# Optimization experiments

Hardware: AMD Instinct MI355X
Metric: run time of the kernel (lower is better)

Reference implementation:

```python
import jax, jax.numpy as jnp
import numpy as np

EPS = 1e-7
N_CAPS_J = 24
ROUTE_MIN = 0.0
N_ITER = 3
INV_TEMP = 0.5
INV_TEMP_DELTA = 0.1


def create_coords_mat(batch, d, h, w, ch, matrix_dim, rel_center=True):
    # Coordinate addition: pad (d,h,w) grid coords to matrix_dim (zeros first).
    subs = (d // 2, h // 2, w // 2) if rel_center else (0, 0, 0)
    f32 = jnp.float32
    dd = jnp.broadcast_to(jnp.arange(d, dtype=f32).reshape(d, 1, 1, 1, 1), (d, h, w, ch, 1)) - subs[0]
    hh = jnp.broadcast_to(jnp.arange(h, dtype=f32).reshape(1, h, 1, 1, 1), (d, h, w, ch, 1)) - subs[1]
    ww = jnp.broadcast_to(jnp.arange(w, dtype=f32).reshape(1, 1, w, 1, 1), (d, h, w, ch, 1)) - subs[2]
    c = jnp.concatenate([dd, hh, ww], -1).reshape(1, d * h * w, ch, 3)
    c = jnp.broadcast_to(c, (batch, d * h * w, ch, 3))
    zeros = jnp.zeros((batch, d * h * w, ch, matrix_dim - 3), dtype=f32)
    return jnp.concatenate([zeros, c], -1)  # (B, dhw, ch, matrix_dim)


def em_routing(v, a_i, beta_v, beta_a):
    # v: (B, Ci, Cj, M) votes; a_i: (B, Ci, 1) input activations.
    B, Ci, Cj, M = v.shape
    a_i = a_i[..., None]  # (B, Ci, 1, 1)

    def stats(r):
        den = r.sum(1, keepdims=True) + EPS                                   # (B,1,Cj,1)
        m = (v * r).sum(1, keepdims=True) / (den + EPS)                       # (B,1,Cj,M)
        s = (r * jnp.square(v - m)).sum(1, keepdims=True) / (den + EPS)       # (B,1,Cj,M)
        cost = ((beta_v + jnp.log(jnp.sqrt(s + EPS) + EPS)) * den).sum(-1, keepdims=True)  # (B,1,Cj,1)
        cm = cost.mean(-2, keepdims=True)
        cs = jnp.sqrt(jnp.square(cost - cm).sum(-2, keepdims=True) / Cj + EPS)
        return m, s, cost, cm, cs

    # Initialization step (uniform assignment scaled by input activations).
    r0 = jnp.full((B, Ci, Cj, 1), 1.0 / Cj, dtype=v.dtype) * a_i
    m, s, cost, cm, cs = stats(r0)
    a_j = jax.nn.sigmoid(INV_TEMP * (beta_a + (cm - cost) / (cs + EPS)))      # (B,1,Cj,1)

    def route(carry, counter):
        mean, stdsqr, act_j, it = carry
        # E-step: Gaussian log-likelihood of each vote under each output capsule.
        expo = (jnp.square(v - mean) / (2.0 * stdsqr + EPS)).sum(-1)          # (B,Ci,Cj)
        coef = -0.5 * jnp.log(2.0 * np.pi * stdsqr + EPS).sum(-1)             # (B,1,Cj)
        log_ap = jnp.log(act_j + EPS).reshape(B, 1, Cj) + coef - expo
        r_ij = jax.nn.softmax(log_ap + EPS, axis=-1)[..., None] * a_i         # (B,Ci,Cj,1)
        # M-step
        m, s, cost, cm, cs = stats(r_ij)
        it = it + counter * INV_TEMP_DELTA
        act = jax.nn.sigmoid(it * (beta_a + (cm - cost) / (cs + EPS)))
        return (m, s, act, it), None

    counters = jnp.arange(1, N_ITER, dtype=v.dtype)  # while_loop runs for counter=1..n_iterations-1
    init = (m, s, a_j, jnp.asarray(INV_TEMP, v.dtype))
    (mean, _, act_j, _), _ = jax.lax.scan(route, init, counters)
    return mean.reshape(B, Cj, M), act_j.reshape(B, Cj, 1)


def setup_inputs() -> dict:
    key = jax.random.key(0)
    k1, k2, k3, k4, k5 = jax.random.split(key, 5)
    B, D, H, W, Ch, M = 4, 4, 14, 14, 32, 16
    J = N_CAPS_J
    pose = jax.random.normal(k1, (B, D, H, W, Ch, M), dtype=jnp.float32)
    activation = jax.random.uniform(k2, (B, D, H, W, Ch, 1), dtype=jnp.float32)
    w = 0.1 * jax.random.normal(k3, (Ch, J, 4, 4), dtype=jnp.float32)
    beta_v = 0.1 * jax.random.normal(k4, (J, M), dtype=jnp.float32)
    beta_a = 0.1 * jax.random.normal(k5, (J, 1), dtype=jnp.float32)
    return {"pose": pose, "activation": activation, "w": w, "beta_v": beta_v, "beta_a": beta_a}


def reference(pose, activation, w, beta_v, beta_a):
    B, D, H, W, Ch, M = pose.shape
    n_i = D * H * W
    sq = int(np.sqrt(M))  # 4x4 pose matrices
    u = pose.reshape(B, n_i, Ch, sq, sq)
    coords = create_coords_mat(B, D, H, W, Ch, M, rel_center=True)            # (B,n_i,Ch,M)
    # Votes: each 4x4 pose matrix times per-(channel, out-capsule) transform.
    votes = jnp.einsum('bicpk,cjkq->bicjpq', u, w).reshape(B, n_i, Ch, N_CAPS_J, M)
    votes = votes + coords[:, :, :, None, :]  # coordinate addition (broadcast over Cj)
    votes = votes.reshape(B, n_i * Ch, N_CAPS_J, M)
    acts = activation.reshape(B, n_i * Ch, 1)
    acts = jnp.where(acts >= ROUTE_MIN, acts, 0.0)
    return em_routing(votes, acts, beta_v, beta_a)
```

## Files before the change

### kernel.cpp

```cpp
#include <hip/hip_runtime.h>
#include <math.h>

#define EPS 1e-7f
#define JC 24
#define CHN 32
#define D_ 4
#define H_ 14
#define W_ 14
#define NI 784
#define CI 25088
#define BATCH 4
#define NP 792
#define ST_STRIDE 792
#define NR 28
#define TWO_PI 6.28318530717958647692f
#define LOG2E 1.44269504088896340736f

__device__ __forceinline__ float groupReduceSum16(float x) {
    x += __shfl_xor(x, 1);
    x += __shfl_xor(x, 2);
    x += __shfl_xor(x, 4);
    x += __shfl_xor(x, 8);
    return x;
}

template<int CTRL>
__device__ __forceinline__ float dpp_mv(float x) {
    return __int_as_float(__builtin_amdgcn_update_dpp(
        0, __float_as_int(x), CTRL, 0xF, 0xF, true));
}

__device__ __forceinline__ float groupSum32_dpp(float x) {
    x += dpp_mv<0xB1>(x);
    x += dpp_mv<0x4E>(x);
    x += dpp_mv<0x141>(x);
    x += dpp_mv<0x140>(x);
    x += __shfl_xor(x, 16);
    return x;
}

template<int PASS, int SPB, int CSEG>
__global__ __launch_bounds__(256, 3)
void accum_kernel(const float* __restrict__ pose, const float* __restrict__ act,
                  const float* __restrict__ w, const float* __restrict__ ST,
                  float* __restrict__ P) {
    __shared__ float w_lds[CSEG * 16 * JC];
    __shared__ float red[4 * JC * 33];

    const int t = threadIdx.x;
    const int h = t >> 5;
    const int jl = t & 31;
    const int jc = jl < 23 ? jl : 23;
    const int b = blockIdx.z;
    const int c0 = blockIdx.y * CSEG;
    const int sp0 = blockIdx.x * SPB;

    for (int idx = t; idx < CSEG * 384; idx += 256) {
        const int cs = idx / 384;
        const int r2 = idx - cs * 384;
        const int jj = r2 >> 4;
        const int kq = r2 & 15;
        w_lds[(cs * 16 + kq) * JC + jj] = w[((size_t)(c0 + cs) * JC + jj) * 16 + kq];
    }

    float SA[16], MS[16], K = 0.f;
    if (PASS) {
        const float* stb = ST + b * ST_STRIDE;
        #pragma unroll
        for (int m4 = 0; m4 < 4; ++m4) {
            float4 a4 = *(const float4*)&stb[jc * 16 + m4 * 4];
            SA[m4*4+0] = a4.x; SA[m4*4+1] = a4.y; SA[m4*4+2] = a4.z; SA[m4*4+3] = a4.w;
            float4 b4 = *(const float4*)&stb[384 + jc * 16 + m4 * 4];
            MS[m4*4+0] = b4.x; MS[m4*4+1] = b4.y; MS[m4*4+2] = b4.z; MS[m4*4+3] = b4.w;
        }
        K = stb[768 + jc];
    }

    float accR = 0.f, accV[16], accV2[16];
    #pragma unroll
    for (int m = 0; m < 16; ++m) { accV[m] = 0.f; accV2[m] = 0.f; }

    __syncthreads();

    #pragma unroll 1
    for (int r = 0; r < SPB / 8; ++r) {
        const int sp = sp0 + r * 8 + h;
        const int dd = sp / (H_ * W_);
        const int rem = sp - dd * (H_ * W_);
        const int hh = rem / W_;
        const int ww = rem - hh * W_;
        const float cd = (float)(dd - D_ / 2);
        const float ch = (float)(hh - H_ / 2);
        const float cw = (float)(ww - W_ / 2);

        const float* upb = pose + (((size_t)b * NI + sp) * CHN + c0) * 16;
        const float* apb = act + ((size_t)b * NI + sp) * CHN + c0;

        float4 pu0 = *(const float4*)(upb + 0);
        float4 pu1 = *(const float4*)(upb + 4);
        float4 pu2 = *(const float4*)(upb + 8);
        float4 pu3 = *(const float4*)(upb + 12);
        float pa = apb[0];

        #pragma unroll 2
        for (int cs = 0; cs < CSEG; ++cs) {
            float4 uu[4] = { pu0, pu1, pu2, pu3 };
            float a = fmaxf(pa, 0.f);

            {
                const int nc = (cs + 1 < CSEG) ? cs + 1 : CSEG - 1;
                const float* upn = upb + nc * 16;
                pu0 = *(const float4*)(upn + 0);
                pu1 = *(const float4*)(upn + 4);
                pu2 = *(const float4*)(upn + 8);
                pu3 = *(const float4*)(upn + 12);
                pa = apb[nc];
            }

            float wv[16];
            #pragma unroll
            for (int kq = 0; kq < 16; ++kq)
                wv[kq] = w_lds[(cs * 16 + kq) * JC + jc];

            float v[16];
            #pragma unroll
            for (int p = 0; p < 4; ++p) {
                const float4 u = uu[p];
                #pragma unroll
                for (int q = 0; q < 4; ++q) {
                    v[p*4+q] = fmaf(u.w, wv[12+q],
                               fmaf(u.z, wv[8+q],
                               fmaf(u.y, wv[4+q], u.x * wv[q])));
                }
            }
            v[13] += cd; v[14] += ch; v[15] += cw;

            float rr;
            if (PASS) {
                float ex0 = 0.f, ex1 = 0.f, ex2 = 0.f, ex3 = 0.f;
                #pragma unroll
                for (int m4 = 0; m4 < 4; ++m4) {
                    float d0 = fmaf(v[m4*4+0], SA[m4*4+0], -MS[m4*4+0]);
                    float d1 = fmaf(v[m4*4+1], SA[m4*4+1], -MS[m4*4+1]);
                    float d2 = fmaf(v[m4*4+2], SA[m4*4+2], -MS[m4*4+2]);
                    float d3 = fmaf(v[m4*4+3], SA[m4*4+3], -MS[m4*4+3]);
                    ex0 = fmaf(d0, d0, ex0);
                    ex1 = fmaf(d1, d1, ex1);
                    ex2 = fmaf(d2, d2, ex2);
                    ex3 = fmaf(d3, d3, ex3);
                }
                float expo = (ex0 + ex1) + (ex2 + ex3);
                float e = (jl < JC) ? exp2f(K - expo) : 0.f;
                float S = groupSum32_dpp(e) + 1e-30f;
                rr = e * a * __frcp_rn(S);
            } else {
                rr = a * (1.0f / 24.0f);
            }

            accR += rr;
            #pragma unroll
            for (int m = 0; m < 16; ++m) {
                accV[m]  = fmaf(rr, v[m], accV[m]);
                accV2[m] = fmaf(rr, v[m] * v[m], accV2[m]);
            }
        }
    }

    accR += __shfl_xor(accR, 32);
    #pragma unroll
    for (int m = 0; m < 16; ++m) {
        accV[m]  += __shfl_xor(accV[m], 32);
        accV2[m] += __shfl_xor(accV2[m], 32);
    }
    const int wid = t >> 6;
    if ((t & 63) < JC) {
        float* rp = &red[(wid * JC + (t & 63)) * 33];
        #pragma unroll
        for (int m = 0; m < 16; ++m) { rp[m] = accV[m]; rp[16 + m] = accV2[m]; }
        rp[32] = accR;
    }
    __syncthreads();

    const int nblkTot = gridDim.x * gridDim.y;
    const int pidx = blockIdx.y * gridDim.x + blockIdx.x;
    float* Pp = P + ((size_t)b * nblkTot + pidx) * NP;
    for (int idx = t; idx < NP; idx += 256) {
        int j, v;
        if (idx < 384)      { j = idx >> 4;        v = idx & 15; }
        else if (idx < 768) { j = (idx-384) >> 4;  v = 16 + ((idx-384) & 15); }
        else                { j = idx - 768;       v = 32; }
        int o = (j * 33) + v;
        float s = red[o] + red[792 + o] + red[2*792 + o] + red[3*792 + o];
        Pp[idx] = s;
    }
}

__global__ __launch_bounds__(256)
void reduce_kernel(const float* __restrict__ P, float* __restrict__ P2,
                   int nblk, int chunk) {
    const int b = blockIdx.y;
    const int r = blockIdx.x;
    const int t = threadIdx.x;
    const int b0 = r * chunk;
    const int b1 = min(b0 + chunk, nblk);
    for (int idx = t; idx < NP; idx += 256) {
        float s = 0.f;
        for (int blk = b0; blk < b1; ++blk)
            s += P[((size_t)b * nblk + blk) * NP + idx];
        P2[((size_t)b * NP + idx) * NR + r] = s;
    }
}

__global__ __launch_bounds__(384)
void stats_kernel(const float* __restrict__ P2, const float* __restrict__ beta_v,
                  const float* __restrict__ beta_a, float* __restrict__ ST,
                  float* __restrict__ out, float it, int final_) {
    __shared__ float red[8];
    const int t = threadIdx.x;
    const int j = t >> 4, m = t & 15;
    const int b = blockIdx.x;
    const int wid = t >> 6, lane = t & 63;

    const float* p2b = P2 + (size_t)b * NP * NR;
    float S1 = 0.f, S2 = 0.f, R = 0.f;
    #pragma unroll
    for (int r4 = 0; r4 < NR; r4 += 4) {
        float4 a = *(const float4*)&p2b[(size_t)t * NR + r4];
        S1 += (a.x + a.y) + (a.z + a.w);
        float4 c = *(const float4*)&p2b[(size_t)(384 + t) * NR + r4];
        S2 += (c.x + c.y) + (c.z + c.w);
        float4 d = *(const float4*)&p2b[(size_t)(768 + j) * NR + r4];
        R += (d.x + d.y) + (d.z + d.w);
    }

    float den  = R + EPS;
    float denp = den + EPS;
    float mean = S1 / denp;
    float s = (S2 - 2.f * mean * S1 + mean * mean * R) / denp;
    s = fmaxf(s, 0.f);

    float c1 = beta_v[j * 16 + m] + logf(sqrtf(s + EPS) + EPS);
    float sc = groupReduceSum16(c1);
    float cost = den * sc;

    float t4 = cost + __shfl_xor(cost, 16);
    t4 += __shfl_xor(t4, 32);
    __syncthreads();
    if (lane == 0) red[wid] = t4;
    __syncthreads();
    float tot = red[0] + red[1] + red[2] + red[3] + red[4] + red[5];
    float cm = tot / 24.f;

    float d2 = cost - cm; d2 *= d2;
    float t4b = d2 + __shfl_xor(d2, 16);
    t4b += __shfl_xor(t4b, 32);
    __syncthreads();
    if (lane == 0) red[wid] = t4b;
    __syncthreads();
    float tot2 = red[0] + red[1] + red[2] + red[3] + red[4] + red[5];
    float cs = sqrtf(tot2 / 24.f + EPS);

    float x = it * (beta_a[j] + (cm - cost) / (cs + EPS));
    float aj = 1.f / (1.f + expf(-x));

    float coef = -0.5f * groupReduceSum16(logf(TWO_PI * s + EPS));

    float Aq = LOG2E / (2.f * s + EPS);
    float SAq = sqrtf(Aq);

    float* stb = ST + b * ST_STRIDE;
    stb[t]       = SAq;
    stb[384 + t] = mean * SAq;
    if (m == 0) stb[768 + j] = (logf(aj + EPS) + coef) * LOG2E;

    if (final_) {
        out[(b * 24 + j) * 16 + m] = mean;
        if (m == 0) out[1536 + b * 24 + j] = aj;
    }
}

template<int SPB, int CSEG>
static void run_all(int spblk, int cblk,
                    const float* pose, const float* act, const float* w,
                    const float* beta_v, const float* beta_a,
                    float* P, float* P2, float* ST, float* out, hipStream_t stream) {
    dim3 agrid(spblk, cblk, BATCH), ablock(256);
    dim3 rgrid(NR, BATCH), rblock(256);
    dim3 sgrid(BATCH), sblock(384);
    const int nblk = spblk * cblk;
    const int chunk = (nblk + NR - 1) / NR;

    accum_kernel<0, SPB, CSEG><<<agrid, ablock, 0, stream>>>(pose, act, w, ST, P);
    reduce_kernel<<<rgrid, rblock, 0, stream>>>(P, P2, nblk, chunk);
    stats_kernel<<<sgrid, sblock, 0, stream>>>(P2, beta_v, beta_a, ST, out, 0.5f, 0);

    accum_kernel<1, SPB, CSEG><<<agrid, ablock, 0, stream>>>(pose, act, w, ST, P);
    reduce_kernel<<<rgrid, rblock, 0, stream>>>(P, P2, nblk, chunk);
    stats_kernel<<<sgrid, sblock, 0, stream>>>(P2, beta_v, beta_a, ST, out, 0.6f, 0);

    accum_kernel<1, SPB, CSEG><<<agrid, ablock, 0, stream>>>(pose, act, w, ST, P);
    reduce_kernel<<<rgrid, rblock, 0, stream>>>(P, P2, nblk, chunk);
    stats_kernel<<<sgrid, sblock, 0, stream>>>(P2, beta_v, beta_a, ST, out, 0.8f, 1);
}

extern "C" void kernel_launch(void* const* d_in, const int* in_sizes, int n_in,
                              void* d_out, int out_size, void* d_ws, size_t ws_size,
                              hipStream_t stream) {
    const float* pose   = (const float*)d_in[0];
    const float* act    = (const float*)d_in[1];
    const float* w      = (const float*)d_in[2];
    const float* beta_v = (const float*)d_in[3];
    const float* beta_a = (const float*)d_in[4];
    float* out = (float*)d_out;
    float* W   = (float*)d_ws;

    const size_t p2_elems = (size_t)BATCH * NP * NR;
    const size_t st_elems = (size_t)BATCH * ST_STRIDE;
    auto need = [&](int spblk, int cblk) -> size_t {
        return ((size_t)BATCH * spblk * cblk * NP + p2_elems + st_elems) * 4;
    };

    if (need(98, 2) <= ws_size) {
        float* P  = W;
        float* P2 = W + (size_t)BATCH * 98 * 2 * NP;
        float* ST = P2 + p2_elems;
        run_all<8, 16>(98, 2, pose, act, w, beta_v, beta_a, P, P2, ST, out, stream);
    } else if (need(49, 2) <= ws_size) {
        float* P  = W;
        float* P2 = W + (size_t)BATCH * 49 * 2 * NP;
        float* ST = P2 + p2_elems;
        run_all<16, 16>(49, 2, pose, act, w, beta_v, beta_a, P, P2, ST, out, stream);
    } else {
        float* P  = W;
        float* P2 = W + (size_t)BATCH * 7 * 1 * NP;
        float* ST = P2 + p2_elems;
        run_all<112, 32>(7, 1, pose, act, w, beta_v, beta_a, P, P2, ST, out, stream);
    }
}
```

Measured before the change: 106.4 us.

## Drop reduce kernel; stats reads transposed partials directly, vectorize w LDS loads

The accumulation kernel now writes its per-block partials transposed (element-major, block-minor), so the stats kernel can sum all 196 block partials per element directly. This removes the intermediate reduce kernel and its launch in each of the three routing iterations. The weight tile in LDS is also re-laid out so each thread reads float2 pairs, halving LDS load instructions. The cost is that a single 4-block stats kernel now performs a longer serial reduction, and the accum stores become strided scatter writes.

Result: slower. 210.0 us (+97.4%).

```diff
diff --git a/kernel.cpp b/kernel.cpp
--- a/kernel.cpp
+++ b/kernel.cpp
@@ -12,7 +12,6 @@
 #define BATCH 4
 #define NP 792
 #define ST_STRIDE 792
-#define NR 28
 #define TWO_PI 6.28318530717958647692f
 #define LOG2E 1.44269504088896340736f
 
@@ -60,7 +59,9 @@
         const int r2 = idx - cs * 384;
         const int jj = r2 >> 4;
         const int kq = r2 & 15;
-        w_lds[(cs * 16 + kq) * JC + jj] = w[((size_t)(c0 + cs) * JC + jj) * 16 + kq];
+        const int k2 = kq >> 1, q2 = kq & 1;
+        w_lds[((cs * 8 + k2) * JC + jj) * 2 + q2] =
+            w[((size_t)(c0 + cs) * JC + jj) * 16 + kq];
     }
 
     float SA[16], MS[16], K = 0.f;
@@ -119,8 +120,11 @@
 
             float wv[16];
             #pragma unroll
-            for (int kq = 0; kq < 16; ++kq)
-                wv[kq] = w_lds[(cs * 16 + kq) * JC + jc];
+            for (int k2 = 0; k2 < 8; ++k2) {
+                float2 t2 = *(const float2*)&w_lds[((cs * 8 + k2) * JC + jc) * 2];
+                wv[k2 * 2 + 0] = t2.x;
+                wv[k2 * 2 + 1] = t2.y;
+            }
 
             float v[16];
             #pragma unroll
@@ -183,7 +187,6 @@
 
     const int nblkTot = gridDim.x * gridDim.y;
     const int pidx = blockIdx.y * gridDim.x + blockIdx.x;
-    float* Pp = P + ((size_t)b * nblkTot + pidx) * NP;
     for (int idx = t; idx < NP; idx += 256) {
         int j, v;
         if (idx < 384)      { j = idx >> 4;        v = idx & 15; }
@@ -191,47 +194,35 @@
         else                { j = idx - 768;       v = 32; }
         int o = (j * 33) + v;
         float s = red[o] + red[792 + o] + red[2*792 + o] + red[3*792 + o];
-        Pp[idx] = s;
-    }
-}
-
-__global__ __launch_bounds__(256)
-void reduce_kernel(const float* __restrict__ P, float* __restrict__ P2,
-                   int nblk, int chunk) {
-    const int b = blockIdx.y;
-    const int r = blockIdx.x;
-    const int t = threadIdx.x;
-    const int b0 = r * chunk;
-    const int b1 = min(b0 + chunk, nblk);
-    for (int idx = t; idx < NP; idx += 256) {
-        float s = 0.f;
-        for (int blk = b0; blk < b1; ++blk)
-            s += P[((size_t)b * nblk + blk) * NP + idx];
-        P2[((size_t)b * NP + idx) * NR + r] = s;
+        P[((size_t)b * NP + idx) * nblkTot + pidx] = s;
     }
 }
 
 __global__ __launch_bounds__(384)
-void stats_kernel(const float* __restrict__ P2, const float* __restrict__ beta_v,
+void stats_kernel(const float* __restrict__ P, const float* __restrict__ beta_v,
                   const float* __restrict__ beta_a, float* __restrict__ ST,
-                  float* __restrict__ out, float it, int final_) {
+                  float* __restrict__ out, int nblk, float it, int final_) {
     __shared__ float red[8];
     const int t = threadIdx.x;
     const int j = t >> 4, m = t & 15;
     const int b = blockIdx.x;
     const int wid = t >> 6, lane = t & 63;
 
-    const float* p2b = P2 + (size_t)b * NP * NR;
+    const float* pb = P + (size_t)b * NP * nblk;
+    const float* p1 = pb + (size_t)t * nblk;
+    const float* p2 = pb + (size_t)(384 + t) * nblk;
+    const float* p3 = pb + (size_t)(768 + j) * nblk;
     float S1 = 0.f, S2 = 0.f, R = 0.f;
-    #pragma unroll
-    for (int r4 = 0; r4 < NR; r4 += 4) {
-        float4 a = *(const float4*)&p2b[(size_t)t * NR + r4];
+    int r4 = 0;
+    for (; r4 + 3 < nblk; r4 += 4) {
+        float4 a = *(const float4*)(p1 + r4);
         S1 += (a.x + a.y) + (a.z + a.w);
-        float4 c = *(const float4*)&p2b[(size_t)(384 + t) * NR + r4];
+        float4 c = *(const float4*)(p2 + r4);
         S2 += (c.x + c.y) + (c.z + c.w);
-        float4 d = *(const float4*)&p2b[(size_t)(768 + j) * NR + r4];
+        float4 d = *(const float4*)(p3 + r4);
         R += (d.x + d.y) + (d.z + d.w);
     }
+    for (; r4 < nblk; ++r4) { S1 += p1[r4]; S2 += p2[r4]; R += p3[r4]; }
 
     float den  = R + EPS;
     float denp = den + EPS;
@@ -283,24 +274,19 @@
 static void run_all(int spblk, int cblk,
                     const float* pose, const float* act, const float* w,
                     const float* beta_v, const float* beta_a,
-                    float* P, float* P2, float* ST, float* out, hipStream_t stream) {
+                    float* P, float* ST, float* out, hipStream_t stream) {
     dim3 agrid(spblk, cblk, BATCH), ablock(256);
-    dim3 rgrid(NR, BATCH), rblock(256);
     dim3 sgrid(BATCH), sblock(384);
     const int nblk = spblk * cblk;
-    const int chunk = (nblk + NR - 1) / NR;
 
     accum_kernel<0, SPB, CSEG><<<agrid, ablock, 0, stream>>>(pose, act, w, ST, P);
-    reduce_kernel<<<rgrid, rblock, 0, stream>>>(P, P2, nblk, chunk);
-    stats_kernel<<<sgrid, sblock, 0, stream>>>(P2, beta_v, beta_a, ST, out, 0.5f, 0);
+    stats_kernel<<<sgrid, sblock, 0, stream>>>(P, beta_v, beta_a, ST, out, nblk, 0.5f, 0);
 
     accum_kernel<1, SPB, CSEG><<<agrid, ablock, 0, stream>>>(pose, act, w, ST, P);
-    reduce_kernel<<<rgrid, rblock, 0, stream>>>(P, P2, nblk, chunk);
-    stats_kernel<<<sgrid, sblock, 0, stream>>>(P2, beta_v, beta_a, ST, out, 0.6f, 0);
+    stats_kernel<<<sgrid, sblock, 0, stream>>>(P, beta_v, beta_a, ST, out, nblk, 0.6f, 0);
 
     accum_kernel<1, SPB, CSEG><<<agrid, ablock, 0, stream>>>(pose, act, w, ST, P);
-    reduce_kernel<<<rgrid, rblock, 0, stream>>>(P, P2, nblk, chunk);
-    stats_kernel<<<sgrid, sblock, 0, stream>>>(P2, beta_v, beta_a, ST, out, 0.8f, 1);
+    stats_kernel<<<sgrid, sblock, 0, stream>>>(P, beta_v, beta_a, ST, out, nblk, 0.8f, 1);
 }
 
 extern "C" void kernel_launch(void* const* d_in, const int* in_sizes, int n_in,
@@ -314,26 +300,22 @@
     float* out = (float*)d_out;
     float* W   = (float*)d_ws;
 
-    const size_t p2_elems = (size_t)BATCH * NP * NR;
     const size_t st_elems = (size_t)BATCH * ST_STRIDE;
     auto need = [&](int spblk, int cblk) -> size_t {
-        return ((size_t)BATCH * spblk * cblk * NP + p2_elems + st_elems) * 4;
+        return ((size_t)BATCH * NP * spblk * cblk + st_elems) * 4;
     };
 
     if (need(98, 2) <= ws_size) {
         float* P  = W;
-        float* P2 = W + (size_t)BATCH * 98 * 2 * NP;
-        float* ST = P2 + p2_elems;
-        run_all<8, 16>(98, 2, pose, act, w, beta_v, beta_a, P, P2, ST, out, stream);
-    } else if (need(49, 2) <= ws_size) {
+        float* ST = W + (size_t)BATCH * NP * 98 * 2;
+        run_all<8, 16>(98, 2, pose, act, w, beta_v, beta_a, P, ST, out, stream);
+    } else if (need(49, 1) <= ws_size) {
         float* P  = W;
-        float* P2 = W + (size_t)BATCH * 49 * 2 * NP;
-        float* ST = P2 + p2_elems;
-        run_all<16, 16>(49, 2, pose, act, w, beta_v, beta_a, P, P2, ST, out, stream);
+        float* ST = W + (size_t)BATCH * NP * 49;
+        run_all<16, 32>(49, 1, pose, act, w, beta_v, beta_a, P, ST, out, stream);
     } else {
         float* P  = W;
-        float* P2 = W + (size_t)BATCH * 7 * 1 * NP;
-        float* ST = P2 + p2_elems;
-        run_all<112, 32>(7, 1, pose, act, w, beta_v, beta_a, P, P2, ST, out, stream);
-    }
-}
+        float* ST = W + (size_t)BATCH * NP * 7;
+        run_all<112, 32>(7, 1, pose, act, w, beta_v, beta_a, P, ST, out, stream);
+    }
+}
```
